# Performance work log

Hardware: AMD Instinct MI355X
Metric: run time of the kernel (lower is better)

The kernel has to match this reference:

```python
import jax, jax.numpy as jnp
import numpy as np

N_STREAMS = 4
DIM = 256
TMAX = 20
RMS_EPS = 1e-05
SK_EPS = 1e-08


def sinkhorn_knopp(logits):
    # logits: [B, T, n, n]; tmax fixed iterations of row/col normalization
    x = logits.astype(jnp.float32)
    x = x - jnp.max(x, axis=(-2, -1), keepdims=True)
    x = jnp.exp(x)
    for _ in range(TMAX):
        x = x / (jnp.sum(x, axis=-2, keepdims=True) + SK_EPS)
        x = x / (jnp.sum(x, axis=-1, keepdims=True) + SK_EPS)
    return x.astype(logits.dtype)


def setup_inputs() -> dict:
    key = jax.random.key(0)
    ks = jax.random.split(key, 5)
    B, T, n, C = 8, 4096, N_STREAMS, DIM
    nc = n * C
    x_streams = jax.random.normal(ks[0], (B, T, n, C), dtype=jnp.float32)
    scale = jnp.ones((nc,), dtype=jnp.float32)
    lim = 1.0 / np.sqrt(nc)
    w_pre = jax.random.uniform(ks[1], (n, nc), minval=-lim, maxval=lim, dtype=jnp.float32)
    w_post = jax.random.uniform(ks[2], (n, nc), minval=-lim, maxval=lim, dtype=jnp.float32)
    w_res = jax.random.uniform(ks[3], (n * n, nc), minval=-lim, maxval=lim, dtype=jnp.float32)
    return {
        "x_streams": x_streams,
        "scale": scale,
        "w_pre": w_pre,
        "w_post": w_post,
        "w_res": w_res,
        "alpha_pre": jnp.float32(0.01),
        "alpha_post": jnp.float32(0.01),
        "alpha_res": jnp.float32(0.01),
        "b_pre": jnp.zeros((n,), dtype=jnp.float32),
        "b_post": jnp.zeros((n,), dtype=jnp.float32),
        "b_res": jnp.zeros((n * n,), dtype=jnp.float32),
    }


def reference(x_streams, scale, w_pre, w_post, w_res,
              alpha_pre, alpha_post, alpha_res, b_pre, b_post, b_res):
    B, T, n, C = x_streams.shape
    x_flat = x_streams.reshape(B, T, n * C)
    # RMSNorm over flattened stream dim
    rms = jnp.mean(x_flat * x_flat, axis=-1, keepdims=True)
    x_norm = x_flat * jax.lax.rsqrt(rms + RMS_EPS) * scale
    # routing projections (Linear with no bias == x @ W.T)
    h_pre = jax.nn.sigmoid(alpha_pre * (x_norm @ w_pre.T) + b_pre)          # [B,T,n]
    h_post = 2.0 * jax.nn.sigmoid(alpha_post * (x_norm @ w_post.T) + b_post)  # [B,T,n]
    h_res = (alpha_res * (x_norm @ w_res.T) + b_res).reshape(B, T, n, n)
    h_res = sinkhorn_knopp(h_res)
    # mixing
    x_in = jnp.einsum('btn,btnc->btc', h_pre, x_streams)   # pre-mix (residual = Identity)
    y = x_in
    resmix = jnp.einsum('btij,btjc->btic', h_res, x_streams)
    addy = h_post[..., None] * y[..., None, :]
    return resmix + addy
```

## Files before the change

kernel.cpp:

```cpp
#include <hip/hip_runtime.h>
#include <math.h>

#define G 8

__device__ __forceinline__ float sigmoidf_(float s) {
    return 1.0f / (1.0f + __expf(-s));
}

__device__ __forceinline__ float fold_(float X, float Y, int m, int l) {
    const bool hi = (l & m) != 0;
    const float a = hi ? Y : X;
    const float b = hi ? X : Y;
    return a + __shfl_xor(b, m);
}

__device__ __forceinline__ void gll16(const float4* g, float* lds) {
    __builtin_amdgcn_global_load_lds(
        (const __attribute__((address_space(1))) void*)g,
        (__attribute__((address_space(3))) void*)lds, 16, 0, 0);
}

__global__ __launch_bounds__(256)
__attribute__((amdgpu_waves_per_eu(2, 2)))
void fused_route_mix(const float* __restrict__ x,
                     const float* __restrict__ scale,
                     const float* __restrict__ w_pre,
                     const float* __restrict__ w_post,
                     const float* __restrict__ w_res,
                     const float* __restrict__ ap_p,
                     const float* __restrict__ apo_p,
                     const float* __restrict__ ar_p,
                     const float* __restrict__ b_pre,
                     const float* __restrict__ b_post,
                     const float* __restrict__ b_res,
                     float* __restrict__ out,
                     int rounds)
{
    __shared__ __align__(16) float xs[2][G * 1024];
    __shared__ __align__(16) float hraw[G * 24];
    __shared__ float sslds[G];

    const int t = threadIdx.x;
    const int w = t >> 6;
    const int l = t & 63;

    float wreg[6][16];
    {
        float scl[16];
        #pragma unroll
        for (int mp = 0; mp < 4; ++mp)
            #pragma unroll
            for (int j = 0; j < 4; ++j)
                scl[4 * mp + j] = scale[4 * l + 256 * mp + j];
        #pragma unroll
        for (int rr = 0; rr < 6; ++rr) {
            const int k = 6 * w + rr;
            const float* wp = (k < 4) ? (w_pre + (size_t)k * 1024)
                            : (k < 8) ? (w_post + (size_t)(k - 4) * 1024)
                                      : (w_res + (size_t)(k - 8) * 1024);
            #pragma unroll
            for (int mp = 0; mp < 4; ++mp)
                #pragma unroll
                for (int j = 0; j < 4; ++j)
                    wreg[rr][4 * mp + j] = wp[4 * l + 256 * mp + j] * scl[4 * mp + j];
        }
    }

    const float a_pre = ap_p[0], a_post = apo_p[0], a_res = ar_p[0];
    float bp[4], bpo[4], br[16];
    #pragma unroll
    for (int k = 0; k < 4; ++k) { bp[k] = b_pre[k]; bpo[k] = b_post[k]; }
    #pragma unroll
    for (int k = 0; k < 16; ++k) br[k] = b_res[k];

    const int rstep = gridDim.x;
    int cur = 0;

    {
        const float4* __restrict__ xg =
            (const float4*)(x + (size_t)blockIdx.x * (G * 1024));
        #pragma unroll
        for (int i = 0; i < G; ++i)
            gll16(xg + i * 256 + (w << 6) + l, &xs[0][i * 1024 + (w << 8)]);
    }

    for (int r = blockIdx.x; r < rounds; r += rstep) {
        const size_t base = (size_t)r * (G * 1024);

        __syncthreads();

        const int rn = r + rstep;
        if (rn < rounds) {
            const float4* __restrict__ xg =
                (const float4*)(x + (size_t)rn * (G * 1024));
            #pragma unroll
            for (int i = 0; i < G; ++i)
                gll16(xg + i * 256 + (w << 6) + l, &xs[cur ^ 1][i * 1024 + (w << 8)]);
        }

        const float* __restrict__ xb = xs[cur];

        for (int i = 0; i < G; ++i) {
            float p0 = 0.f, p1 = 0.f, p2 = 0.f, p3 = 0.f, p4 = 0.f, p5 = 0.f;
            float ss = 0.f;
            const float4* __restrict__ xi4 = (const float4*)(xb + i * 1024);
            #pragma unroll
            for (int mp = 0; mp < 4; ++mp) {
                const float4 xv = xi4[l + 64 * mp];
                const float xe[4] = {xv.x, xv.y, xv.z, xv.w};
                #pragma unroll
                for (int j = 0; j < 4; ++j) {
                    const float xj = xe[j];
                    p0 = fmaf(xj, wreg[0][4 * mp + j], p0);
                    p1 = fmaf(xj, wreg[1][4 * mp + j], p1);
                    p2 = fmaf(xj, wreg[2][4 * mp + j], p2);
                    p3 = fmaf(xj, wreg[3][4 * mp + j], p3);
                    p4 = fmaf(xj, wreg[4][4 * mp + j], p4);
                    p5 = fmaf(xj, wreg[5][4 * mp + j], p5);
                    ss = fmaf(xj, xj, ss);
                }
            }
            const float q0 = fold_(p0, p1, 32, l);
            const float q1 = fold_(p2, p3, 32, l);
            const float q2 = fold_(p4, p5, 32, l);
            const float q3 = ss + __shfl_xor(ss, 32);
            const float r0v = fold_(q0, q1, 16, l);
            const float r1v = fold_(q2, q3, 16, l);
            float s = fold_(r0v, r1v, 8, l);
            s += __shfl_xor(s, 4);
            s += __shfl_xor(s, 2);
            s += __shfl_xor(s, 1);
            if ((l & 7) == 0) {
                const int vid = ((l >> 3) & 1) * 4 + ((l >> 4) & 1) * 2 + ((l >> 5) & 1);
                if (vid < 6) hraw[i * 24 + 6 * w + vid] = s;
                else if (w == 0 && vid == 6) sslds[i] = s;
            }
        }

        asm volatile("s_waitcnt lgkmcnt(0)\n\ts_barrier" ::: "memory");

        float Mw0, Mw1, Mw2, Mw3;
        {
            const int tk = l & (G - 1);
            const float inv = rsqrtf(sslds[tk] * (1.0f / 1024.0f) + 1e-5f);
            float hr[24];
            const float4* __restrict__ hp = (const float4*)(hraw + tk * 24);
            #pragma unroll
            for (int q = 0; q < 6; ++q) {
                const float4 hv = hp[q];
                hr[4 * q + 0] = hv.x; hr[4 * q + 1] = hv.y;
                hr[4 * q + 2] = hv.z; hr[4 * q + 3] = hv.w;
            }

            float hpre[4], hpost[4];
            #pragma unroll
            for (int j = 0; j < 4; ++j)
                hpre[j] = sigmoidf_(fmaf(a_pre * inv, hr[j], bp[j]));
            #pragma unroll
            for (int i = 0; i < 4; ++i)
                hpost[i] = 2.0f * sigmoidf_(fmaf(a_post * inv, hr[4 + i], bpo[i]));

            float K[4][4];
            float mx = -1e30f;
            #pragma unroll
            for (int i = 0; i < 4; ++i)
                #pragma unroll
                for (int j = 0; j < 4; ++j) {
                    const float vv = fmaf(a_res * inv, hr[8 + 4 * i + j], br[4 * i + j]);
                    K[i][j] = vv;
                    mx = fmaxf(mx, vv);
                }
            #pragma unroll
            for (int i = 0; i < 4; ++i)
                #pragma unroll
                for (int j = 0; j < 4; ++j)
                    K[i][j] = __expf(K[i][j] - mx);

            float u[4] = {1.f, 1.f, 1.f, 1.f};
            float v[4] = {1.f, 1.f, 1.f, 1.f};
            for (int it = 0; it < 20; ++it) {
                #pragma unroll
                for (int j = 0; j < 4; ++j) {
                    const float S = u[0] * K[0][j] + u[1] * K[1][j]
                                  + u[2] * K[2][j] + u[3] * K[3][j];
                    v[j] = v[j] * __builtin_amdgcn_rcpf(fmaf(v[j], S, 1e-8f));
                }
                #pragma unroll
                for (int i = 0; i < 4; ++i) {
                    const float T = K[i][0] * v[0] + K[i][1] * v[1]
                                  + K[i][2] * v[2] + K[i][3] * v[3];
                    u[i] = u[i] * __builtin_amdgcn_rcpf(fmaf(u[i], T, 1e-8f));
                }
            }

            const float uw  = (w == 0) ? u[0] : (w == 1) ? u[1] : (w == 2) ? u[2] : u[3];
            const float hpw = (w == 0) ? hpost[0] : (w == 1) ? hpost[1]
                            : (w == 2) ? hpost[2] : hpost[3];
            #define KW(j) ((w == 0) ? K[0][j] : (w == 1) ? K[1][j] : (w == 2) ? K[2][j] : K[3][j])
            Mw0 = fmaf(uw * KW(0), v[0], hpw * hpre[0]);
            Mw1 = fmaf(uw * KW(1), v[1], hpw * hpre[1]);
            Mw2 = fmaf(uw * KW(2), v[2], hpw * hpre[2]);
            Mw3 = fmaf(uw * KW(3), v[3], hpw * hpre[3]);
            #undef KW
        }

        for (int i = 0; i < G; ++i) {
            const float m0 = __shfl(Mw0, i);
            const float m1 = __shfl(Mw1, i);
            const float m2 = __shfl(Mw2, i);
            const float m3 = __shfl(Mw3, i);
            const float4* __restrict__ xt = (const float4*)(xb + i * 1024);
            const float4 a0 = xt[0 * 64 + l];
            const float4 a1 = xt[1 * 64 + l];
            const float4 a2 = xt[2 * 64 + l];
            const float4 a3 = xt[3 * 64 + l];
            float4 o;
            o.x = m0 * a0.x + m1 * a1.x + m2 * a2.x + m3 * a3.x;
            o.y = m0 * a0.y + m1 * a1.y + m2 * a2.y + m3 * a3.y;
            o.z = m0 * a0.z + m1 * a1.z + m2 * a2.z + m3 * a3.z;
            o.w = m0 * a0.w + m1 * a1.w + m2 * a2.w + m3 * a3.w;
            ((float4*)(out + base))[i * 256 + (w << 6) + l] = o;
        }

        cur ^= 1;
    }
}

extern "C" void kernel_launch(void* const* d_in, const int* in_sizes, int n_in,
                              void* d_out, int out_size, void* d_ws, size_t ws_size,
                              hipStream_t stream) {
    const float* x      = (const float*)d_in[0];
    const float* scale  = (const float*)d_in[1];
    const float* w_pre  = (const float*)d_in[2];
    const float* w_post = (const float*)d_in[3];
    const float* w_res  = (const float*)d_in[4];
    const float* a_pre  = (const float*)d_in[5];
    const float* a_post = (const float*)d_in[6];
    const float* a_res  = (const float*)d_in[7];
    const float* b_pre  = (const float*)d_in[8];
    const float* b_post = (const float*)d_in[9];
    const float* b_res  = (const float*)d_in[10];
    float* out = (float*)d_out;

    const int tokens = in_sizes[0] / 1024;
    const int rounds = tokens / G;
    const int grid = rounds < 512 ? rounds : 512;

    fused_route_mix<<<grid, 256, 0, stream>>>(
        x, scale, w_pre, w_post, w_res,
        a_pre, a_post, a_res, b_pre, b_post, b_res,
        out, rounds);
}
```

Before: 293.0 us.

## Double block size to 512 threads, split projections across 8 waves, single-wave Sinkhorn

Doubles the block to 8 waves, so each wave holds 3 projection weight rows instead of 6. This halves register pressure and lets occupancy rise to 4 waves per EU. The Sinkhorn routing solve now runs only in wave 0. It writes the full 4x4 mixing matrices for the 8 tokens to LDS, and an extra barrier then lets all waves do the mix stage split by token halves. This aims to cut redundant Sinkhorn work across waves and raise latency hiding, at the cost of an additional block barrier and serial work in a single wave while the others wait.

```diff
diff --git a/kernel.cpp b/kernel.cpp
--- a/kernel.cpp
+++ b/kernel.cpp
@@ -14,14 +14,14 @@
     return a + __shfl_xor(b, m);
 }
 
-__device__ __forceinline__ void gll16(const float4* g, float* lds) {
+__device__ __forceinline__ void gll16(const float4* g, const float* lds) {
     __builtin_amdgcn_global_load_lds(
         (const __attribute__((address_space(1))) void*)g,
         (__attribute__((address_space(3))) void*)lds, 16, 0, 0);
 }
 
-__global__ __launch_bounds__(256)
-__attribute__((amdgpu_waves_per_eu(2, 2)))
+__global__ __launch_bounds__(512)
+__attribute__((amdgpu_waves_per_eu(4, 4)))
 void fused_route_mix(const float* __restrict__ x,
                      const float* __restrict__ scale,
                      const float* __restrict__ w_pre,
@@ -39,39 +39,26 @@
     __shared__ __align__(16) float xs[2][G * 1024];
     __shared__ __align__(16) float hraw[G * 24];
     __shared__ float sslds[G];
+    __shared__ __align__(16) float Mlds[G * 16];
 
     const int t = threadIdx.x;
     const int w = t >> 6;
     const int l = t & 63;
 
-    float wreg[6][16];
-    {
-        float scl[16];
+    float wreg[3][16];
+    #pragma unroll
+    for (int rr = 0; rr < 3; ++rr) {
+        const int k = 3 * w + rr;
+        const float* wp = (k < 4) ? (w_pre + (size_t)k * 1024)
+                        : (k < 8) ? (w_post + (size_t)(k - 4) * 1024)
+                                  : (w_res + (size_t)(k - 8) * 1024);
         #pragma unroll
         for (int mp = 0; mp < 4; ++mp)
             #pragma unroll
             for (int j = 0; j < 4; ++j)
-                scl[4 * mp + j] = scale[4 * l + 256 * mp + j];
-        #pragma unroll
-        for (int rr = 0; rr < 6; ++rr) {
-            const int k = 6 * w + rr;
-            const float* wp = (k < 4) ? (w_pre + (size_t)k * 1024)
-                            : (k < 8) ? (w_post + (size_t)(k - 4) * 1024)
-                                      : (w_res + (size_t)(k - 8) * 1024);
-            #pragma unroll
-            for (int mp = 0; mp < 4; ++mp)
-                #pragma unroll
-                for (int j = 0; j < 4; ++j)
-                    wreg[rr][4 * mp + j] = wp[4 * l + 256 * mp + j] * scl[4 * mp + j];
-        }
+                wreg[rr][4 * mp + j] =
+                    wp[4 * l + 256 * mp + j] * scale[4 * l + 256 * mp + j];
     }
-
-    const float a_pre = ap_p[0], a_post = apo_p[0], a_res = ar_p[0];
-    float bp[4], bpo[4], br[16];
-    #pragma unroll
-    for (int k = 0; k < 4; ++k) { bp[k] = b_pre[k]; bpo[k] = b_post[k]; }
-    #pragma unroll
-    for (int k = 0; k < 16; ++k) br[k] = b_res[k];
 
     const int rstep = gridDim.x;
     int cur = 0;
@@ -80,8 +67,8 @@
         const float4* __restrict__ xg =
             (const float4*)(x + (size_t)blockIdx.x * (G * 1024));
         #pragma unroll
-        for (int i = 0; i < G; ++i)
-            gll16(xg + i * 256 + (w << 6) + l, &xs[0][i * 1024 + (w << 8)]);
+        for (int i = 0; i < 4; ++i)
+            gll16(xg + i * 512 + t, &xs[0][i * 2048 + (w << 8)]);
     }
 
     for (int r = blockIdx.x; r < rounds; r += rstep) {
@@ -94,15 +81,15 @@
             const float4* __restrict__ xg =
                 (const float4*)(x + (size_t)rn * (G * 1024));
             #pragma unroll
-            for (int i = 0; i < G; ++i)
-                gll16(xg + i * 256 + (w << 6) + l, &xs[cur ^ 1][i * 1024 + (w << 8)]);
+            for (int i = 0; i < 4; ++i)
+                gll16(xg + i * 512 + t, &xs[cur ^ 1][i * 2048 + (w << 8)]);
         }
 
         const float* __restrict__ xb = xs[cur];
 
+        #pragma unroll 2
         for (int i = 0; i < G; ++i) {
-            float p0 = 0.f, p1 = 0.f, p2 = 0.f, p3 = 0.f, p4 = 0.f, p5 = 0.f;
-            float ss = 0.f;
+            float p0 = 0.f, p1 = 0.f, p2 = 0.f, ss = 0.f;
             const float4* __restrict__ xi4 = (const float4*)(xb + i * 1024);
             #pragma unroll
             for (int mp = 0; mp < 4; ++mp) {
@@ -114,33 +101,26 @@
                     p0 = fmaf(xj, wreg[0][4 * mp + j], p0);
                     p1 = fmaf(xj, wreg[1][4 * mp + j], p1);
                     p2 = fmaf(xj, wreg[2][4 * mp + j], p2);
-                    p3 = fmaf(xj, wreg[3][4 * mp + j], p3);
-                    p4 = fmaf(xj, wreg[4][4 * mp + j], p4);
-                    p5 = fmaf(xj, wreg[5][4 * mp + j], p5);
                     ss = fmaf(xj, xj, ss);
                 }
             }
             const float q0 = fold_(p0, p1, 32, l);
-            const float q1 = fold_(p2, p3, 32, l);
-            const float q2 = fold_(p4, p5, 32, l);
-            const float q3 = ss + __shfl_xor(ss, 32);
-            const float r0v = fold_(q0, q1, 16, l);
-            const float r1v = fold_(q2, q3, 16, l);
-            float s = fold_(r0v, r1v, 8, l);
+            const float q1 = fold_(p2, ss, 32, l);
+            float s = fold_(q0, q1, 16, l);
+            s += __shfl_xor(s, 8);
             s += __shfl_xor(s, 4);
             s += __shfl_xor(s, 2);
             s += __shfl_xor(s, 1);
-            if ((l & 7) == 0) {
-                const int vid = ((l >> 3) & 1) * 4 + ((l >> 4) & 1) * 2 + ((l >> 5) & 1);
-                if (vid < 6) hraw[i * 24 + 6 * w + vid] = s;
-                else if (w == 0 && vid == 6) sslds[i] = s;
+            if ((l & 15) == 0) {
+                const int vid = ((l >> 5) & 1) | (((l >> 4) & 1) << 1);
+                if (vid < 3) hraw[i * 24 + 3 * w + vid] = s;
+                else if (w == 0) sslds[i] = s;
             }
         }
 
         asm volatile("s_waitcnt lgkmcnt(0)\n\ts_barrier" ::: "memory");
 
-        float Mw0, Mw1, Mw2, Mw3;
-        {
+        if (w == 0) {
             const int tk = l & (G - 1);
             const float inv = rsqrtf(sslds[tk] * (1.0f / 1024.0f) + 1e-5f);
             float hr[24];
@@ -151,14 +131,15 @@
                 hr[4 * q + 0] = hv.x; hr[4 * q + 1] = hv.y;
                 hr[4 * q + 2] = hv.z; hr[4 * q + 3] = hv.w;
             }
+            const float a_pre = ap_p[0], a_post = apo_p[0], a_res = ar_p[0];
 
             float hpre[4], hpost[4];
             #pragma unroll
             for (int j = 0; j < 4; ++j)
-                hpre[j] = sigmoidf_(fmaf(a_pre * inv, hr[j], bp[j]));
-            #pragma unroll
-            for (int i = 0; i < 4; ++i)
-                hpost[i] = 2.0f * sigmoidf_(fmaf(a_post * inv, hr[4 + i], bpo[i]));
+                hpre[j] = sigmoidf_(fmaf(a_pre * inv, hr[j], b_pre[j]));
+            #pragma unroll
+            for (int i = 0; i < 4; ++i)
+                hpost[i] = 2.0f * sigmoidf_(fmaf(a_post * inv, hr[4 + i], b_post[i]));
 
             float K[4][4];
             float mx = -1e30f;
@@ -166,7 +147,7 @@
             for (int i = 0; i < 4; ++i)
                 #pragma unroll
                 for (int j = 0; j < 4; ++j) {
-                    const float vv = fmaf(a_res * inv, hr[8 + 4 * i + j], br[4 * i + j]);
+                    const float vv = fmaf(a_res * inv, hr[8 + 4 * i + j], b_res[4 * i + j]);
                     K[i][j] = vv;
                     mx = fmaxf(mx, vv);
                 }
@@ -181,45 +162,51 @@
             for (int it = 0; it < 20; ++it) {
                 #pragma unroll
                 for (int j = 0; j < 4; ++j) {
-                    const float S = u[0] * K[0][j] + u[1] * K[1][j]
-                                  + u[2] * K[2][j] + u[3] * K[3][j];
+                    const float S = (fmaf(u[0], K[0][j], u[1] * K[1][j]))
+                                  + (fmaf(u[2], K[2][j], u[3] * K[3][j]));
                     v[j] = v[j] * __builtin_amdgcn_rcpf(fmaf(v[j], S, 1e-8f));
                 }
                 #pragma unroll
                 for (int i = 0; i < 4; ++i) {
-                    const float T = K[i][0] * v[0] + K[i][1] * v[1]
-                                  + K[i][2] * v[2] + K[i][3] * v[3];
+                    const float T = (fmaf(K[i][0], v[0], K[i][1] * v[1]))
+                                  + (fmaf(K[i][2], v[2], K[i][3] * v[3]));
                     u[i] = u[i] * __builtin_amdgcn_rcpf(fmaf(u[i], T, 1e-8f));
                 }
             }
 
-            const float uw  = (w == 0) ? u[0] : (w == 1) ? u[1] : (w == 2) ? u[2] : u[3];
-            const float hpw = (w == 0) ? hpost[0] : (w == 1) ? hpost[1]
-                            : (w == 2) ? hpost[2] : hpost[3];
-            #define KW(j) ((w == 0) ? K[0][j] : (w == 1) ? K[1][j] : (w == 2) ? K[2][j] : K[3][j])
-            Mw0 = fmaf(uw * KW(0), v[0], hpw * hpre[0]);
-            Mw1 = fmaf(uw * KW(1), v[1], hpw * hpre[1]);
-            Mw2 = fmaf(uw * KW(2), v[2], hpw * hpre[2]);
-            Mw3 = fmaf(uw * KW(3), v[3], hpw * hpre[3]);
-            #undef KW
-        }
-
-        for (int i = 0; i < G; ++i) {
-            const float m0 = __shfl(Mw0, i);
-            const float m1 = __shfl(Mw1, i);
-            const float m2 = __shfl(Mw2, i);
-            const float m3 = __shfl(Mw3, i);
+            if (l < G) {
+                float4* Md = (float4*)(Mlds + (l << 4));
+                #pragma unroll
+                for (int i2 = 0; i2 < 4; ++i2) {
+                    float4 row;
+                    row.x = fmaf(u[i2] * K[i2][0], v[0], hpost[i2] * hpre[0]);
+                    row.y = fmaf(u[i2] * K[i2][1], v[1], hpost[i2] * hpre[1]);
+                    row.z = fmaf(u[i2] * K[i2][2], v[2], hpost[i2] * hpre[2]);
+                    row.w = fmaf(u[i2] * K[i2][3], v[3], hpost[i2] * hpre[3]);
+                    Md[i2] = row;
+                }
+            }
+        }
+
+        asm volatile("s_waitcnt lgkmcnt(0)\n\ts_barrier" ::: "memory");
+
+        const int w4 = w & 3;
+        const int half = t >> 8;
+        #pragma unroll
+        for (int ii = 0; ii < 4; ++ii) {
+            const int i = 2 * ii + half;
+            const float4 m4 = ((const float4*)Mlds)[(i << 2) + w4];
             const float4* __restrict__ xt = (const float4*)(xb + i * 1024);
             const float4 a0 = xt[0 * 64 + l];
             const float4 a1 = xt[1 * 64 + l];
             const float4 a2 = xt[2 * 64 + l];
             const float4 a3 = xt[3 * 64 + l];
             float4 o;
-            o.x = m0 * a0.x + m1 * a1.x + m2 * a2.x + m3 * a3.x;
-            o.y = m0 * a0.y + m1 * a1.y + m2 * a2.y + m3 * a3.y;
-            o.z = m0 * a0.z + m1 * a1.z + m2 * a2.z + m3 * a3.z;
-            o.w = m0 * a0.w + m1 * a1.w + m2 * a2.w + m3 * a3.w;
-            ((float4*)(out + base))[i * 256 + (w << 6) + l] = o;
+            o.x = m4.x * a0.x + m4.y * a1.x + m4.z * a2.x + m4.w * a3.x;
+            o.y = m4.x * a0.y + m4.y * a1.y + m4.z * a2.y + m4.w * a3.y;
+            o.z = m4.x * a0.z + m4.y * a1.z + m4.z * a2.z + m4.w * a3.z;
+            o.w = m4.x * a0.w + m4.y * a1.w + m4.z * a2.w + m4.w * a3.w;
+            ((float4*)(out + base))[(i << 8) + (w4 << 6) + l] = o;
         }
 
         cur ^= 1;
@@ -246,7 +233,7 @@
     const int rounds = tokens / G;
     const int grid = rounds < 512 ? rounds : 512;
 
-    fused_route_mix<<<grid, 256, 0, stream>>>(
+    fused_route_mix<<<grid, 512, 0, stream>>>(
         x, scale, w_pre, w_post, w_res,
         a_pre, a_post, a_res, b_pre, b_post, b_res,
         out, rounds);
```

Result: faster. 282.9 us (-3.4%).
